# Kernel tuning notes

Measured on AMD Instinct MI355X. Metric: run time of the kernel, lower is better.

## Reference

```python
import jax, jax.numpy as jnp
import numpy as np


def setup_inputs() -> dict:
    key = jax.random.key(0)
    k1, k2, k3 = jax.random.split(key, 3)
    bs, S, d, C = 2, 196, 512, 1006
    imgFeaturemap = jax.random.normal(k1, (bs, S, d), dtype=jnp.float32)
    wordFeatures = jax.random.normal(k2, (C, d), dtype=jnp.float32)
    fc3_w = jax.random.normal(k3, (d, d), dtype=jnp.float32) * 0.02
    fc3_b = jnp.zeros((d,), dtype=jnp.float32)
    return {"imgFeaturemap": imgFeaturemap, "wordFeatures": wordFeatures,
            "fc3_w": fc3_w, "fc3_b": fc3_b}


def reference(imgFeaturemap, wordFeatures, fc3_w, fc3_b):
    # imgFeaturemap: (bs, S, d); wordFeatures: (C, d)
    # Broadcast multiply + tanh: (bs, S, C, d)
    t = jnp.tanh(imgFeaturemap[:, :, None, :] * wordFeatures[None, None, :, :])
    # Per-row Linear (PyTorch Linear: x @ W^T + b)
    feat = jnp.einsum('bscd,ed->bsce', t, fc3_w) + fc3_b
    # Softmax over spatial axis S (axis=1), independently per (class, channel)
    coef = jax.nn.softmax(feat, axis=1)
    # Softmax-weighted spatial pooling per class: (bs, C, d)
    semanticFeature = jnp.einsum('bsd,bscd->bcd', imgFeaturemap, coef)
    return semanticFeature
```

## Files before the change

### kernel.cpp

```cpp
#include <hip/hip_runtime.h>

using half8   = __attribute__((ext_vector_type(8))) _Float16;
using floatx4 = __attribute__((ext_vector_type(4))) float;

namespace {
constexpr int S = 196, D = 512, C = 1006, Cpad = 1024;
constexpr int CB = 16;
constexpr int EBLK = 256;
constexpr int BK = 64;
constexpr int TPB = 256;
constexpr int SCH = 3;
constexpr int RS = 64;
constexpr float KTANH = 2.885390082f;
constexpr float INVK  = 0.34657359028f;
constexpr float LOG2E = 1.44269504f;

constexpr size_t W16_BYTES = (size_t)D * D * 2;
constexpr size_t LA_OFF    = W16_BYTES;
constexpr size_t SLICE_ELEMS = (size_t)2 * Cpad * D;
constexpr size_t SL_BYTES  = (size_t)SCH * SLICE_ELEMS * 4;
constexpr size_t SLICE_NEED = LA_OFF + 2 * SL_BYTES;
constexpr size_t L_BYTES   = SLICE_ELEMS * 4;

__device__ __forceinline__ int sw_off(int row, int seg) {
    return row * RS + ((seg ^ (row & 7)) << 3);
}

__device__ __forceinline__ void gload16(const _Float16* g, _Float16* l) {
    __builtin_amdgcn_global_load_lds(
        (const __attribute__((address_space(1))) unsigned int*)g,
        (__attribute__((address_space(3))) unsigned int*)l, 16, 0, 0);
}

__device__ __forceinline__ _Float16 tanh_ps(float y) {
    float e = __builtin_amdgcn_exp2f(y);
    return (_Float16)(1.0f - 2.0f * __builtin_amdgcn_rcpf(e + 1.0f));
}

__global__ void prep_w16sw(const float* __restrict__ fw, _Float16* __restrict__ W16sw) {
    int id = blockIdx.x * blockDim.x + threadIdx.x;
    int kki = id >> 12;
    int r   = (id >> 3) & 511;
    int j   = id & 7;
    const float* src = fw + (size_t)r * D + kki * BK + j * 8;
    floatx4 v0 = *(const floatx4*)src;
    floatx4 v1 = *(const floatx4*)(src + 4);
    half8 h;
    h[0] = (_Float16)(v0[0] * LOG2E); h[1] = (_Float16)(v0[1] * LOG2E);
    h[2] = (_Float16)(v0[2] * LOG2E); h[3] = (_Float16)(v0[3] * LOG2E);
    h[4] = (_Float16)(v1[0] * LOG2E); h[5] = (_Float16)(v1[1] * LOG2E);
    h[6] = (_Float16)(v1[2] * LOG2E); h[7] = (_Float16)(v1[3] * LOG2E);
    *(half8*)&W16sw[((size_t)kki << 15) + r * RS + ((j ^ (r & 7)) << 3)] = h;
}

__global__ __launch_bounds__(TPB, 3) void semdec_mfma(
    const float* __restrict__ img, const float* __restrict__ word,
    const _Float16* __restrict__ W16sw,
    float* __restrict__ lbase, float* __restrict__ abase, int use_slice)
{
    __shared__ __align__(16) _Float16 Wc[EBLK * RS];
    __shared__ __align__(16) _Float16 Tc[4 * CB * RS];
    __shared__ __align__(16) float imgS[4][D];

    const int ct = blockIdx.x;
    const int et = blockIdx.y & 1;
    const int b  = blockIdx.y >> 1;
    const int sc = blockIdx.z;

    const int tid  = threadIdx.x;
    const int lane = tid & 63;
    const int wv   = tid >> 6;
    const int l15  = lane & 15;
    const int quad = lane >> 4;

    const int c0 = ct * CB;
    const int e0 = et * EBLK;

    const int siB  = tid >> 7;
    const int ciT  = (tid & 127) >> 3;
    const int segT = tid & 7;
    int cgT = c0 + ciT; if (cgT > C - 1) cgT = C - 1;
    const float* wordRowT = word + (size_t)cgT * D + segT * 8;

    floatx4 lacc[4], aacc[4];
    #pragma unroll
    for (int ej = 0; ej < 4; ++ej) {
        lacc[ej] = (floatx4){0.f, 0.f, 0.f, 0.f};
        aacc[ej] = (floatx4){0.f, 0.f, 0.f, 0.f};
    }

    const float* imgB = img + (size_t)b * S * D;
    const int s_base = sc * 66;
    const int npass = (sc < 2) ? 17 : 16;

    floatx4 wc0 = *(const floatx4*)(wordRowT);
    floatx4 wc1 = *(const floatx4*)(wordRowT + 4);

    for (int pr = 0; pr < npass; ++pr) {
        const int s0 = s_base + pr * 4;
        const int slim = (pr == 16) ? 2 : 4;

        __syncthreads();
        #pragma unroll
        for (int it = 0; it < 2; ++it) {
            int sid = it * TPB + tid;
            int si = sid >> 7, pos = (sid & 127) << 2;
            floatx4 v = *(const floatx4*)&imgB[(size_t)(s0 + si) * D + pos];
            floatx4 sv = {v[0] * KTANH, v[1] * KTANH, v[2] * KTANH, v[3] * KTANH};
            *(floatx4*)&imgS[si][pos] = sv;
        }

        floatx4 acc[4][4];
        #pragma unroll
        for (int si = 0; si < 4; ++si)
            #pragma unroll
            for (int ej = 0; ej < 4; ++ej)
                acc[si][ej] = (floatx4){0.f, 0.f, 0.f, 0.f};

        for (int kk = 0; kk < D; kk += BK) {
            const int kki = kk >> 6;
            __syncthreads();
            {
                const _Float16* wg = W16sw + ((size_t)kki << 15) + ((size_t)e0 << 6);
                #pragma unroll
                for (int it = 0; it < 8; ++it) {
                    int o = ((wv * 8 + it) << 9) + (lane << 3);
                    gload16(wg + o, &Wc[o]);
                }
            }
            #pragma unroll
            for (int it = 0; it < 2; ++it) {
                int si = it * 2 + siB;
                const float* ip = &imgS[si][kk + segT * 8];
                floatx4 i0 = *(const floatx4*)ip;
                floatx4 i1 = *(const floatx4*)(ip + 4);
                half8 t;
                t[0] = tanh_ps(i0[0] * wc0[0]); t[1] = tanh_ps(i0[1] * wc0[1]);
                t[2] = tanh_ps(i0[2] * wc0[2]); t[3] = tanh_ps(i0[3] * wc0[3]);
                t[4] = tanh_ps(i1[0] * wc1[0]); t[5] = tanh_ps(i1[1] * wc1[1]);
                t[6] = tanh_ps(i1[2] * wc1[2]); t[7] = tanh_ps(i1[3] * wc1[3]);
                *(half8*)&Tc[sw_off(si * CB + ciT, segT)] = t;
            }
            __syncthreads();

            const int knext = (kk + BK) & (D - 1);
            floatx4 wn0 = *(const floatx4*)(wordRowT + knext);
            floatx4 wn1 = *(const floatx4*)(wordRowT + knext + 4);

            #pragma unroll
            for (int k2 = 0; k2 < 2; ++k2) {
                const int jb = (k2 << 2) + quad;
                half8 bf[4], af[4];
                #pragma unroll
                for (int ej = 0; ej < 4; ++ej)
                    bf[ej] = *(const half8*)&Wc[sw_off(wv * 64 + ej * 16 + l15, jb)];
                #pragma unroll
                for (int si = 0; si < 4; ++si)
                    af[si] = *(const half8*)&Tc[sw_off(si * CB + l15, jb)];
                #pragma unroll
                for (int si = 0; si < 4; ++si)
                    #pragma unroll
                    for (int ej = 0; ej < 4; ++ej)
                        acc[si][ej] = __builtin_amdgcn_mfma_f32_16x16x32_f16(
                            af[si], bf[ej], acc[si][ej], 0, 0, 0);
            }
            wc0 = wn0; wc1 = wn1;
        }
        #pragma unroll
        for (int si = 0; si < 4; ++si) {
            if (si >= slim) break;
            #pragma unroll
            for (int ej = 0; ej < 4; ++ej) {
                float ie = imgS[si][e0 + wv * 64 + ej * 16 + l15] * INVK;
                #pragma unroll
                for (int r = 0; r < 4; ++r) {
                    float ev = __builtin_amdgcn_exp2f(acc[si][ej][r]);
                    lacc[ej][r] += ev;
                    aacc[ej][r] += ie * ev;
                }
            }
        }
    }

    if (use_slice) {
        float* lsl = lbase + (size_t)sc * SLICE_ELEMS;
        float* asl = abase + (size_t)sc * SLICE_ELEMS;
        #pragma unroll
        for (int r = 0; r < 4; ++r) {
            int cg = c0 + quad * 4 + r;
            #pragma unroll
            for (int ej = 0; ej < 4; ++ej) {
                int eg = e0 + wv * 64 + ej * 16 + l15;
                size_t o = ((size_t)b * Cpad + cg) * D + eg;
                lsl[o] = lacc[ej][r];
                asl[o] = aacc[ej][r];
            }
        }
    } else {
        #pragma unroll
        for (int r = 0; r < 4; ++r) {
            int cg = c0 + quad * 4 + r;
            #pragma unroll
            for (int ej = 0; ej < 4; ++ej) {
                int eg = e0 + wv * 64 + ej * 16 + l15;
                atomicAdd(&lbase[((size_t)b * Cpad + cg) * D + eg], lacc[ej][r]);
                if (cg < C)
                    atomicAdd(&abase[((size_t)b * C + cg) * D + eg], aacc[ej][r]);
            }
        }
    }
}

__global__ void finalize_k(const float* __restrict__ lbase, const float* __restrict__ abase,
                           float* __restrict__ out, int use_slice) {
    int o = blockIdx.x * blockDim.x + threadIdx.x;
    if (o >= 2 * C * D) return;
    int b = o / (C * D);
    int rem = o - b * (C * D);
    int c = rem >> 9;
    int e = rem & (D - 1);
    size_t p = ((size_t)b * Cpad + c) * D + e;
    if (use_slice) {
        float l = 0.f, a = 0.f;
        #pragma unroll
        for (int scn = 0; scn < SCH; ++scn) {
            l += lbase[(size_t)scn * SLICE_ELEMS + p];
            a += abase[(size_t)scn * SLICE_ELEMS + p];
        }
        out[o] = a / l;
    } else {
        out[o] = out[o] / lbase[p];
    }
}

}

extern "C" void kernel_launch(void* const* d_in, const int* in_sizes, int n_in,
                              void* d_out, int out_size, void* d_ws, size_t ws_size,
                              hipStream_t stream) {
    const float* img  = (const float*)d_in[0];
    const float* word = (const float*)d_in[1];
    const float* fw   = (const float*)d_in[2];
    float* out = (float*)d_out;
    char* ws = (char*)d_ws;

    _Float16* W16sw = (_Float16*)ws;
    const int use_slice = (ws_size >= SLICE_NEED) ? 1 : 0;

    hipLaunchKernelGGL(prep_w16sw, dim3(128), dim3(256), 0, stream, fw, W16sw);

    float *lbase, *abase;
    if (use_slice) {
        lbase = (float*)(ws + LA_OFF);
        abase = (float*)(ws + LA_OFF + SL_BYTES);
    } else {
        lbase = (float*)(ws + LA_OFF);
        abase = out;
        hipMemsetAsync(lbase, 0, L_BYTES, stream);
        hipMemsetAsync(out, 0, (size_t)2 * C * D * 4, stream);
    }

    hipLaunchKernelGGL(semdec_mfma, dim3(64, 4, SCH), dim3(TPB), 0, stream,
                       img, word, W16sw, lbase, abase, use_slice);

    hipLaunchKernelGGL(finalize_k, dim3((2 * C * D + 255) / 256), dim3(256), 0, stream,
                       lbase, abase, out, use_slice);
}
```

Before: 357.7 us.

## Split spatial axis into four chunks with two rows per pass

Cuts the per-pass spatial tile from 4 rows to 2 and splits S across 4 chunks instead of 3, so the grid has more blocks. Launch bounds rise to 4 blocks per CU to match the smaller accumulator and LDS footprint. The aim is better occupancy and load balance across CUs. In exchange, each weight tile staged in LDS now serves half as many MFMAs, so weight traffic per FLOP doubles, and there are more partial slices to reduce afterwards.

```diff
diff --git a/kernel.cpp b/kernel.cpp
--- a/kernel.cpp
+++ b/kernel.cpp
@@ -9,7 +9,8 @@
 constexpr int EBLK = 256;
 constexpr int BK = 64;
 constexpr int TPB = 256;
-constexpr int SCH = 3;
+constexpr int SPP = 2;
+constexpr int SCH = 4;
 constexpr int RS = 64;
 constexpr float KTANH = 2.885390082f;
 constexpr float INVK  = 0.34657359028f;
@@ -53,14 +54,14 @@
     *(half8*)&W16sw[((size_t)kki << 15) + r * RS + ((j ^ (r & 7)) << 3)] = h;
 }
 
-__global__ __launch_bounds__(TPB, 3) void semdec_mfma(
+__global__ __launch_bounds__(TPB, 4) void semdec_mfma(
     const float* __restrict__ img, const float* __restrict__ word,
     const _Float16* __restrict__ W16sw,
     float* __restrict__ lbase, float* __restrict__ abase, int use_slice)
 {
     __shared__ __align__(16) _Float16 Wc[EBLK * RS];
-    __shared__ __align__(16) _Float16 Tc[4 * CB * RS];
-    __shared__ __align__(16) float imgS[4][D];
+    __shared__ __align__(16) _Float16 Tc[SPP * CB * RS];
+    __shared__ __align__(16) float imgS[SPP][D];
 
     const int ct = blockIdx.x;
     const int et = blockIdx.y & 1;
@@ -76,7 +77,7 @@
     const int c0 = ct * CB;
     const int e0 = et * EBLK;
 
-    const int siB  = tid >> 7;
+    const int siT  = tid >> 7;
     const int ciT  = (tid & 127) >> 3;
     const int segT = tid & 7;
     int cgT = c0 + ciT; if (cgT > C - 1) cgT = C - 1;
@@ -90,29 +91,27 @@
     }
 
     const float* imgB = img + (size_t)b * S * D;
-    const int s_base = sc * 66;
-    const int npass = (sc < 2) ? 17 : 16;
+    const int s_base = sc * 49;
 
     floatx4 wc0 = *(const floatx4*)(wordRowT);
     floatx4 wc1 = *(const floatx4*)(wordRowT + 4);
 
-    for (int pr = 0; pr < npass; ++pr) {
-        const int s0 = s_base + pr * 4;
-        const int slim = (pr == 16) ? 2 : 4;
+    for (int pr = 0; pr < 25; ++pr) {
+        const int s0 = s_base + pr * 2;
+        const int slim = (pr == 24) ? 1 : 2;
 
         __syncthreads();
-        #pragma unroll
-        for (int it = 0; it < 2; ++it) {
-            int sid = it * TPB + tid;
-            int si = sid >> 7, pos = (sid & 127) << 2;
-            floatx4 v = *(const floatx4*)&imgB[(size_t)(s0 + si) * D + pos];
+        {
+            int si = tid >> 7, pos = (tid & 127) << 2;
+            int srow = s0 + si; if (srow > S - 1) srow = S - 1;
+            floatx4 v = *(const floatx4*)&imgB[(size_t)srow * D + pos];
             floatx4 sv = {v[0] * KTANH, v[1] * KTANH, v[2] * KTANH, v[3] * KTANH};
             *(floatx4*)&imgS[si][pos] = sv;
         }
 
-        floatx4 acc[4][4];
-        #pragma unroll
-        for (int si = 0; si < 4; ++si)
+        floatx4 acc[SPP][4];
+        #pragma unroll
+        for (int si = 0; si < SPP; ++si)
             #pragma unroll
             for (int ej = 0; ej < 4; ++ej)
                 acc[si][ej] = (floatx4){0.f, 0.f, 0.f, 0.f};
@@ -128,10 +127,8 @@
                     gload16(wg + o, &Wc[o]);
                 }
             }
-            #pragma unroll
-            for (int it = 0; it < 2; ++it) {
-                int si = it * 2 + siB;
-                const float* ip = &imgS[si][kk + segT * 8];
+            {
+                const float* ip = &imgS[siT][kk + segT * 8];
                 floatx4 i0 = *(const floatx4*)ip;
                 floatx4 i1 = *(const floatx4*)(ip + 4);
                 half8 t;
@@ -139,7 +136,7 @@
                 t[2] = tanh_ps(i0[2] * wc0[2]); t[3] = tanh_ps(i0[3] * wc0[3]);
                 t[4] = tanh_ps(i1[0] * wc1[0]); t[5] = tanh_ps(i1[1] * wc1[1]);
                 t[6] = tanh_ps(i1[2] * wc1[2]); t[7] = tanh_ps(i1[3] * wc1[3]);
-                *(half8*)&Tc[sw_off(si * CB + ciT, segT)] = t;
+                *(half8*)&Tc[sw_off(siT * CB + ciT, segT)] = t;
             }
             __syncthreads();
 
@@ -150,15 +147,15 @@
             #pragma unroll
             for (int k2 = 0; k2 < 2; ++k2) {
                 const int jb = (k2 << 2) + quad;
-                half8 bf[4], af[4];
+                half8 bf[4], af[SPP];
                 #pragma unroll
                 for (int ej = 0; ej < 4; ++ej)
                     bf[ej] = *(const half8*)&Wc[sw_off(wv * 64 + ej * 16 + l15, jb)];
                 #pragma unroll
-                for (int si = 0; si < 4; ++si)
+                for (int si = 0; si < SPP; ++si)
                     af[si] = *(const half8*)&Tc[sw_off(si * CB + l15, jb)];
                 #pragma unroll
-                for (int si = 0; si < 4; ++si)
+                for (int si = 0; si < SPP; ++si)
                     #pragma unroll
                     for (int ej = 0; ej < 4; ++ej)
                         acc[si][ej] = __builtin_amdgcn_mfma_f32_16x16x32_f16(
@@ -167,7 +164,7 @@
             wc0 = wn0; wc1 = wn1;
         }
         #pragma unroll
-        for (int si = 0; si < 4; ++si) {
+        for (int si = 0; si < SPP; ++si) {
             if (si >= slim) break;
             #pragma unroll
             for (int ej = 0; ej < 4; ++ej) {
```

Result: slower. 1.024 ms (+186.3%).
